# Kernel optimization log

Measured on AMD Instinct MI355X. Metric: run time of the kernel, lower is better.

## Reference

```python
import jax, jax.numpy as jnp
import numpy as np

U, I, NG, D, G, B = 100000, 50000, 20000, 64, 20, 16384
H_GE = (D + 2 * D) // 2  # 96, group_encoder hidden

def setup_inputs() -> dict:
    key = jax.random.key(0)
    ks = jax.random.split(key, 24)
    s = 0.1
    return {
        'group_inputs': jax.random.randint(ks[0], (B,), 0, NG),
        'item_inputs': jax.random.randint(ks[1], (B,), 0, I),
        'group_members': jax.random.randint(ks[2], (NG, G), 0, U),
        'eps': jax.random.normal(ks[3], (B, D), dtype=jnp.float32),
        'user_emb': jax.random.normal(ks[4], (U, D), dtype=jnp.float32) * s,
        'item_emb': jax.random.normal(ks[5], (I, D), dtype=jnp.float32) * s,
        # user_encoder: MLP(D, D, 1) -> Linear(D,D), ReLU, Linear(D,D)
        'ue_w1': jax.random.normal(ks[6], (D, D), dtype=jnp.float32) * s,
        'ue_b1': jnp.zeros((D,), jnp.float32),
        'ue_w2': jax.random.normal(ks[7], (D, D), dtype=jnp.float32) * s,
        'ue_b2': jnp.zeros((D,), jnp.float32),
        # group_encoder: MLP(D, 2D, 1) -> Linear(D,96), ReLU, Linear(96,2D)
        'ge_w1': jax.random.normal(ks[8], (D, H_GE), dtype=jnp.float32) * s,
        'ge_b1': jnp.zeros((H_GE,), jnp.float32),
        'ge_w2': jax.random.normal(ks[9], (H_GE, 2 * D), dtype=jnp.float32) * s,
        'ge_b2': jnp.zeros((2 * D,), jnp.float32),
        # attention: Linear(2D,16), ReLU, Linear(16,1)
        'at_w1': jax.random.normal(ks[10], (2 * D, 16), dtype=jnp.float32) * s,
        'at_b1': jnp.zeros((16,), jnp.float32),
        'at_w2': jax.random.normal(ks[11], (16, 1), dtype=jnp.float32) * s,
        'at_b2': jnp.zeros((1,), jnp.float32),
        # predict: Linear(3D,8), ReLU, Linear(8,1)
        'pr_w1': jax.random.normal(ks[12], (3 * D, 8), dtype=jnp.float32) * s,
        'pr_b1': jnp.zeros((8,), jnp.float32),
        'pr_w2': jax.random.normal(ks[13], (8, 1), dtype=jnp.float32) * s,
        'pr_b2': jnp.zeros((1,), jnp.float32),
    }

def reference(group_inputs, item_inputs, group_members, eps,
              user_emb, item_emb,
              ue_w1, ue_b1, ue_w2, ue_b2,
              ge_w1, ge_b1, ge_w2, ge_b2,
              at_w1, at_b1, at_w2, at_b2,
              pr_w1, pr_b1, pr_w2, pr_b2):
    mem_idx = group_members[group_inputs]              # [B, G]
    me = user_emb[mem_idx]                             # [B, G, D] gather
    # user encoder MLP
    enc = jnp.maximum(me @ ue_w1 + ue_b1, 0) @ ue_w2 + ue_b2
    gz = jnp.maximum(jnp.mean(enc, axis=1), 0)         # [B, D]
    gz = jnp.maximum(gz @ ge_w1 + ge_b1, 0) @ ge_w2 + ge_b2  # [B, 2D]
    z_mu, log_sigma = gz[:, :D], gz[:, D:]
    z_sigma = 0.1 + 0.9 * jax.nn.sigmoid(log_sigma)
    ie = item_emb[item_inputs]                          # [B, D]
    gi = jnp.concatenate([me, jnp.broadcast_to(ie[:, None, :], me.shape)], axis=-1)  # [B, G, 2D]
    score = jnp.maximum(gi @ at_w1 + at_b1, 0) @ at_w2 + at_b2  # [B, G, 1]
    w = jax.nn.softmax(score[..., 0], axis=1)           # [B, G]
    g_att = jnp.einsum('bg,bgd->bd', w, me)             # [B, D]
    ge_full = g_att + z_mu + z_sigma * eps              # sample_z with given eps
    ncf = jnp.concatenate([ge_full * ie, ge_full, ie], axis=-1)  # [B, 3D]
    h = jnp.maximum(ncf @ pr_w1 + pr_b1, 0) @ pr_w2 + pr_b2
    return jax.nn.sigmoid(h)                            # [B, 1]
```

## Files before the change

kernel.cpp:

```cpp
#include <hip/hip_runtime.h>
#include <hip/hip_bf16.h>
#include <math.h>

#define G_   20
#define BT   16

typedef __attribute__((ext_vector_type(8))) short bf8;
typedef __attribute__((ext_vector_type(4))) float f4;

#define FMB  0
#define FAT  10
#define FUE2 12
#define FGE1 20
#define FGE2 32
#define FPR  56
#define FTOT 62

__device__ __forceinline__ unsigned cvt2(float x, float y){
    float2 f; f.x = x; f.y = y;
    __hip_bfloat162 h = __float22bfloat162_rn(f);
    return *reinterpret_cast<unsigned*>(&h);
}
__device__ __forceinline__ unsigned short cvt1(float x){
    __hip_bfloat16 h = __float2bfloat16(x);
    return *reinterpret_cast<unsigned short*>(&h);
}
__device__ __forceinline__ bf8 pack8(float4 a, float4 b){
    union { bf8 v; unsigned u[4]; } t;
    t.u[0] = cvt2(a.x, a.y); t.u[1] = cvt2(a.z, a.w);
    t.u[2] = cvt2(b.x, b.y); t.u[3] = cvt2(b.z, b.w);
    return t.v;
}

__global__ __launch_bounds__(256) void vargr_prep(
    const float* __restrict__ ue_w1, const float* __restrict__ ue_w2,
    const float* __restrict__ ge_w1, const float* __restrict__ ge_w2,
    const float* __restrict__ at_w1, const float* __restrict__ pr_w1,
    unsigned short* __restrict__ ws)
{
    int f = blockIdx.x * 256 + threadIdx.x;
    if (f >= FTOT * 64) return;
    int lane = f & 63, grp = f >> 6;
    int col = lane & 15;
    int q8  = (lane >> 4) * 8;
    float v[8];
    if (grp < FAT){
        int g = grp - FMB; int nt = g >> 1; int k0 = (g & 1)*32 + q8; int c = nt*16 + col;
        #pragma unroll
        for (int q = 0; q < 8; ++q)
            v[q] = (c < 64) ? ue_w1[(k0+q)*64 + c] : at_w1[(k0+q)*16 + (c - 64)];
    } else if (grp < FUE2){
        int g = grp - FAT; int k0 = g*32 + q8;
        #pragma unroll
        for (int q = 0; q < 8; ++q) v[q] = at_w1[(64 + k0 + q)*16 + col];
    } else if (grp < FGE1){
        int g = grp - FUE2; int nt = g >> 1; int k0 = (g & 1)*32 + q8;
        #pragma unroll
        for (int q = 0; q < 8; ++q) v[q] = ue_w2[(k0+q)*64 + nt*16 + col];
    } else if (grp < FGE2){
        int g = grp - FGE1; int nt = g >> 1; int k0 = (g & 1)*32 + q8;
        #pragma unroll
        for (int q = 0; q < 8; ++q) v[q] = ge_w1[(k0+q)*96 + nt*16 + col];
    } else if (grp < FPR){
        int g = grp - FGE2; int nt = g / 3; int k0 = (g % 3)*32 + q8;
        #pragma unroll
        for (int q = 0; q < 8; ++q) v[q] = ge_w2[(k0+q)*128 + nt*16 + col];
    } else {
        int g = grp - FPR; int k0 = g*32 + q8;
        #pragma unroll
        for (int q = 0; q < 8; ++q) v[q] = (col < 8) ? pr_w1[(k0+q)*8 + col] : 0.f;
    }
    union { bf8 b; unsigned u[4]; } t;
    t.u[0] = cvt2(v[0], v[1]); t.u[1] = cvt2(v[2], v[3]);
    t.u[2] = cvt2(v[4], v[5]); t.u[3] = cvt2(v[6], v[7]);
    *reinterpret_cast<bf8*>(ws + (size_t)f * 8) = t.b;
}

__global__ __launch_bounds__(256, 4) void vargr_main(
    const int*   __restrict__ group_inputs,
    const int*   __restrict__ item_inputs,
    const int*   __restrict__ group_members,
    const float* __restrict__ eps,
    const float* __restrict__ user_emb,
    const float* __restrict__ item_emb,
    const float* __restrict__ ue_b1, const float* __restrict__ ue_b2,
    const float* __restrict__ ge_b1, const float* __restrict__ ge_b2,
    const float* __restrict__ at_b1, const float* __restrict__ at_w2,
    const float* __restrict__ at_b2, const float* __restrict__ pr_b1,
    const float* __restrict__ pr_w2, const float* __restrict__ pr_b2,
    const unsigned short* __restrict__ ws,
    float* __restrict__ out)
{
    __shared__ unsigned short xAh[BT*136];
    __shared__ unsigned short xBh[BT*136];
    __shared__ float ieb[BT*68];
    __shared__ float gefb[BT*64];
    __shared__ float wsm[BT*G_];
    __shared__ int   sidx[BT*G_];
    __shared__ float x3u[BT*132];

    const int tid = threadIdx.x;
    const int w = tid >> 6, l = tid & 63;
    const int lq = l >> 4, lr = l & 15;
    const int bbase = blockIdx.x * BT;
    const bf8* wsf = (const bf8*)ws;

    bf8 bfr[5][2];
    #pragma unroll
    for (int nt = 0; nt < 5; ++nt)
        #pragma unroll
        for (int kt = 0; kt < 2; ++kt)
            bfr[nt][kt] = wsf[(FMB + nt*2 + kt)*64 + l];
    bf8 abot0 = wsf[(FAT + 0)*64 + l];
    bf8 abot1 = wsf[(FAT + 1)*64 + l];

    float bias1[4];
    #pragma unroll
    for (int nt = 0; nt < 4; ++nt) bias1[nt] = ue_b1[nt*16 + lr];
    const float aw2  = at_w2[lr];
    const float atb2 = at_b2[0];

    {
        int bb = 4*w + lq;
        int item = item_inputs[bbase + bb];
        ((float4*)(ieb + bb*68))[lr] = ((const float4*)(item_emb + (size_t)item*64))[lr];
    }
    if (l < G_){
        #pragma unroll
        for (int i = 0; i < 4; ++i){
            int bb = 4*w + i;
            int gid = group_inputs[bbase + bb];
            sidx[bb*G_ + l] = group_members[gid*G_ + l];
        }
    }
    __syncthreads();

    f4 tvacc = (f4){0.f, 0.f, 0.f, 0.f};
    #pragma unroll
    for (int kt = 0; kt < 2; ++kt){
        const float* ap = ieb + lr*68 + kt*32 + lq*8;
        bf8 a = pack8(*(const float4*)ap, *(const float4*)(ap + 4));
        tvacc = __builtin_amdgcn_mfma_f32_16x16x32_bf16(a, kt ? abot1 : abot0, tvacc, 0, 0, 0);
    }
    const float atb1 = at_b1[lr];
    float tvi[4];
    #pragma unroll
    for (int i = 0; i < 4; ++i)
        tvi[i] = __shfl(tvacc[i], w*16 + lr) + atb1;

    float rem[4];
    {
        int sx = sidx[(4*w + (lr >> 2))*G_ + 16 + (lr & 3)];
        const float4* p = (const float4*)(user_emb + (size_t)sx*64) + lq*2;
        bf8 a0 = pack8(p[0], p[1]);
        bf8 a1 = pack8(p[8], p[9]);
        f4 acc[5];
        #pragma unroll
        for (int nt = 0; nt < 5; ++nt) acc[nt] = (f4){0.f, 0.f, 0.f, 0.f};
        #pragma unroll
        for (int nt = 0; nt < 5; ++nt){
            acc[nt] = __builtin_amdgcn_mfma_f32_16x16x32_bf16(a0, bfr[nt][0], acc[nt], 0, 0, 0);
            acc[nt] = __builtin_amdgcn_mfma_f32_16x16x32_bf16(a1, bfr[nt][1], acc[nt], 0, 0, 0);
        }
        #pragma unroll
        for (int nt = 0; nt < 4; ++nt){
            float rs = 0.f;
            #pragma unroll
            for (int rr = 0; rr < 4; ++rr) rs += fmaxf(acc[nt][rr] + bias1[nt], 0.f);
            rem[nt] = rs;
        }
        float tvq = (lq == 0) ? tvi[0] : (lq == 1) ? tvi[1] : (lq == 2) ? tvi[2] : tvi[3];
        float vv[4];
        #pragma unroll
        for (int rr = 0; rr < 4; ++rr) vv[rr] = fmaxf(acc[4][rr] + tvq, 0.f) * aw2;
        #pragma unroll
        for (int rr = 0; rr < 4; ++rr){
            vv[rr] += __shfl_xor(vv[rr], 1, 16);
            vv[rr] += __shfl_xor(vv[rr], 2, 16);
            vv[rr] += __shfl_xor(vv[rr], 4, 16);
            vv[rr] += __shfl_xor(vv[rr], 8, 16);
        }
        if (lr == 0){
            #pragma unroll
            for (int rr = 0; rr < 4; ++rr)
                wsm[(4*w + lq)*G_ + 16 + rr] = vv[rr] + atb2;
        }
    }

    #pragma unroll 1
    for (int i = 0; i < 4; ++i){
        const int bb = 4*w + i;
        const int sx = sidx[bb*G_ + lr];
        const float4* p = (const float4*)(user_emb + (size_t)sx*64) + lq*2;
        bf8 a0 = pack8(p[0], p[1]);
        bf8 a1 = pack8(p[8], p[9]);
        f4 acc[5];
        #pragma unroll
        for (int nt = 0; nt < 5; ++nt) acc[nt] = (f4){0.f, 0.f, 0.f, 0.f};
        #pragma unroll
        for (int nt = 0; nt < 5; ++nt){
            acc[nt] = __builtin_amdgcn_mfma_f32_16x16x32_bf16(a0, bfr[nt][0], acc[nt], 0, 0, 0);
            acc[nt] = __builtin_amdgcn_mfma_f32_16x16x32_bf16(a1, bfr[nt][1], acc[nt], 0, 0, 0);
        }
        #pragma unroll
        for (int nt = 0; nt < 4; ++nt){
            float rs = 0.f;
            #pragma unroll
            for (int rr = 0; rr < 4; ++rr) rs += fmaxf(acc[nt][rr] + bias1[nt], 0.f);
            if (lq == i) rs += rem[nt];
            rs += __shfl_xor(rs, 16);
            rs += __shfl_xor(rs, 32);
            if (lq == nt) xAh[bb*136 + nt*16 + lr] = cvt1(rs * (1.f / G_));
        }
        {
            float vv[4];
            #pragma unroll
            for (int rr = 0; rr < 4; ++rr) vv[rr] = fmaxf(acc[4][rr] + tvi[i], 0.f) * aw2;
            #pragma unroll
            for (int rr = 0; rr < 4; ++rr){
                vv[rr] += __shfl_xor(vv[rr], 1, 16);
                vv[rr] += __shfl_xor(vv[rr], 2, 16);
                vv[rr] += __shfl_xor(vv[rr], 4, 16);
                vv[rr] += __shfl_xor(vv[rr], 8, 16);
            }
            if (lr == 0){
                #pragma unroll
                for (int rr = 0; rr < 4; ++rr)
                    wsm[bb*G_ + 4*lq + rr] = vv[rr] + atb2;
            }
        }
        {
            float sval = (l < G_) ? wsm[bb*G_ + l] : -3.0e38f;
            float mx = sval;
            mx = fmaxf(mx, __shfl_xor(mx, 1, 32));
            mx = fmaxf(mx, __shfl_xor(mx, 2, 32));
            mx = fmaxf(mx, __shfl_xor(mx, 4, 32));
            mx = fmaxf(mx, __shfl_xor(mx, 8, 32));
            mx = fmaxf(mx, __shfl_xor(mx, 16, 32));
            float e = (l < G_) ? expf(sval - mx) : 0.f;
            float sm = e;
            sm += __shfl_xor(sm, 1, 32);
            sm += __shfl_xor(sm, 2, 32);
            sm += __shfl_xor(sm, 4, 32);
            sm += __shfl_xor(sm, 8, 32);
            sm += __shfl_xor(sm, 16, 32);
            if (l < G_) wsm[bb*G_ + l] = e / sm;
        }
        {
            float ga = 0.f;
            #pragma unroll
            for (int g = 0; g < G_; ++g)
                ga += wsm[bb*G_ + g] * user_emb[(size_t)sidx[bb*G_ + g]*64 + l];
            gefb[bb*64 + l] = ga;
        }
    }
    __syncthreads();

    {
        int col = w*16 + lr;
        f4 acc = (f4){0.f, 0.f, 0.f, 0.f};
        #pragma unroll
        for (int kt = 0; kt < 2; ++kt){
            bf8 a = *(const bf8*)(xAh + lr*136 + kt*32 + lq*8);
            acc = __builtin_amdgcn_mfma_f32_16x16x32_bf16(a, wsf[(FUE2 + w*2 + kt)*64 + l], acc, 0, 0, 0);
        }
        float bs = ue_b2[col];
        #pragma unroll
        for (int rr = 0; rr < 4; ++rr)
            xBh[(4*lq + rr)*136 + col] = cvt1(fmaxf(acc[rr] + bs, 0.f));
    }
    __syncthreads();
    for (int t = w; t < 6; t += 4){
        int col = t*16 + lr;
        f4 acc = (f4){0.f, 0.f, 0.f, 0.f};
        #pragma unroll
        for (int kt = 0; kt < 2; ++kt){
            bf8 a = *(const bf8*)(xBh + lr*136 + kt*32 + lq*8);
            acc = __builtin_amdgcn_mfma_f32_16x16x32_bf16(a, wsf[(FGE1 + t*2 + kt)*64 + l], acc, 0, 0, 0);
        }
        float bs = ge_b1[col];
        #pragma unroll
        for (int rr = 0; rr < 4; ++rr)
            xAh[(4*lq + rr)*136 + col] = cvt1(fmaxf(acc[rr] + bs, 0.f));
    }
    __syncthreads();
    for (int t = w; t < 8; t += 4){
        int col = t*16 + lr;
        f4 acc = (f4){0.f, 0.f, 0.f, 0.f};
        #pragma unroll
        for (int kt = 0; kt < 3; ++kt){
            bf8 a = *(const bf8*)(xAh + lr*136 + kt*32 + lq*8);
            acc = __builtin_amdgcn_mfma_f32_16x16x32_bf16(a, wsf[(FGE2 + t*3 + kt)*64 + l], acc, 0, 0, 0);
        }
        float bs = ge_b2[col];
        #pragma unroll
        for (int rr = 0; rr < 4; ++rr)
            x3u[(4*lq + rr)*132 + col] = acc[rr] + bs;
    }
    __syncthreads();

    #pragma unroll
    for (int i = 0; i < 4; ++i){
        int bb = 4*w + i;
        float mu  = x3u[bb*132 + l];
        float sgr = x3u[bb*132 + 64 + l];
        float sg  = 0.1f + 0.9f / (1.f + expf(-sgr));
        gefb[bb*64 + l] += mu + sg * eps[(size_t)(bbase + bb)*64 + l];
    }
    __syncthreads();
    unsigned short* ncf = (unsigned short*)x3u;
    #pragma unroll
    for (int i = 0; i < 4; ++i){
        int bb = 4*w + i;
        float gef = gefb[bb*64 + l];
        float iev = ieb[bb*68 + l];
        ncf[bb*200 + l]       = cvt1(gef * iev);
        ncf[bb*200 + 64 + l]  = cvt1(gef);
        ncf[bb*200 + 128 + l] = cvt1(iev);
    }
    __syncthreads();
    if (w == 0){
        f4 acc = (f4){0.f, 0.f, 0.f, 0.f};
        #pragma unroll
        for (int kt = 0; kt < 6; ++kt){
            bf8 a = *(const bf8*)(ncf + lr*200 + kt*32 + lq*8);
            acc = __builtin_amdgcn_mfma_f32_16x16x32_bf16(a, wsf[(FPR + kt)*64 + l], acc, 0, 0, 0);
        }
        float pb1 = (lr < 8) ? pr_b1[lr] : 0.f;
        float pw2 = (lr < 8) ? pr_w2[lr] : 0.f;
        float pb2 = pr_b2[0];
        float vv[4];
        #pragma unroll
        for (int rr = 0; rr < 4; ++rr) vv[rr] = fmaxf(acc[rr] + pb1, 0.f) * pw2;
        #pragma unroll
        for (int rr = 0; rr < 4; ++rr){
            vv[rr] += __shfl_xor(vv[rr], 1, 16);
            vv[rr] += __shfl_xor(vv[rr], 2, 16);
            vv[rr] += __shfl_xor(vv[rr], 4, 16);
            vv[rr] += __shfl_xor(vv[rr], 8, 16);
        }
        if (lr == 0){
            #pragma unroll
            for (int rr = 0; rr < 4; ++rr)
                out[bbase + 4*lq + rr] = 1.f / (1.f + expf(-(vv[rr] + pb2)));
        }
    }
}

extern "C" void kernel_launch(void* const* d_in, const int* in_sizes, int n_in,
                              void* d_out, int out_size, void* d_ws, size_t ws_size,
                              hipStream_t stream) {
    const int*   group_inputs  = (const int*)d_in[0];
    const int*   item_inputs   = (const int*)d_in[1];
    const int*   group_members = (const int*)d_in[2];
    const float* eps           = (const float*)d_in[3];
    const float* user_emb      = (const float*)d_in[4];
    const float* item_emb      = (const float*)d_in[5];
    const float* ue_w1 = (const float*)d_in[6];
    const float* ue_b1 = (const float*)d_in[7];
    const float* ue_w2 = (const float*)d_in[8];
    const float* ue_b2 = (const float*)d_in[9];
    const float* ge_w1 = (const float*)d_in[10];
    const float* ge_b1 = (const float*)d_in[11];
    const float* ge_w2 = (const float*)d_in[12];
    const float* ge_b2 = (const float*)d_in[13];
    const float* at_w1 = (const float*)d_in[14];
    const float* at_b1 = (const float*)d_in[15];
    const float* at_w2 = (const float*)d_in[16];
    const float* at_b2 = (const float*)d_in[17];
    const float* pr_w1 = (const float*)d_in[18];
    const float* pr_b1 = (const float*)d_in[19];
    const float* pr_w2 = (const float*)d_in[20];
    const float* pr_b2 = (const float*)d_in[21];
    float* out = (float*)d_out;
    unsigned short* ws = (unsigned short*)d_ws;

    vargr_prep<<<(FTOT*64 + 255)/256, 256, 0, stream>>>(
        ue_w1, ue_w2, ge_w1, ge_w2, at_w1, pr_w1, ws);

    const int nb = in_sizes[0];
    vargr_main<<<nb / BT, 256, 0, stream>>>(
        group_inputs, item_inputs, group_members, eps, user_emb, item_emb,
        ue_b1, ue_b2, ge_b1, ge_b2, at_b1, at_w2, at_b2, pr_b1, pr_w2, pr_b2,
        ws, out);
}
```

Baseline: 44.97 us.

## Double block tile to 32 rows and run tail MLP per-wave without barriers

Each block now handles 32 batch rows with 512 threads instead of 16 rows with 256 threads. After the gather and attention phase, only two waves continue, and each owns a 16-row slice. That wave runs the ue2, ge1, ge2, sampling and predict MLP chain alone, so the block-wide __syncthreads between tail stages go away, and eps is prefetched into registers early. The cost is that six of eight waves sit idle during the tail and register pressure rises. The diff also relies on the unseen shared-memory arrays being resized for BT=32.

```diff
diff --git a/kernel.cpp b/kernel.cpp
--- a/kernel.cpp
+++ b/kernel.cpp
@@ -3,7 +3,7 @@
 #include <math.h>
 
 #define G_   20
-#define BT   16
+#define BT   32
 
 typedef __attribute__((ext_vector_type(8))) short bf8;
 typedef __attribute__((ext_vector_type(4))) float f4;
@@ -76,7 +76,7 @@
     *reinterpret_cast<bf8*>(ws + (size_t)f * 8) = t.b;
 }
 
-__global__ __launch_bounds__(256, 4) void vargr_main(
+__global__ __launch_bounds__(512, 4) void vargr_main(
     const int*   __restrict__ group_inputs,
     const int*   __restrict__ item_inputs,
     const int*   __restrict__ group_members,
@@ -136,17 +136,20 @@
     __syncthreads();
 
     f4 tvacc = (f4){0.f, 0.f, 0.f, 0.f};
-    #pragma unroll
-    for (int kt = 0; kt < 2; ++kt){
-        const float* ap = ieb + lr*68 + kt*32 + lq*8;
-        bf8 a = pack8(*(const float4*)ap, *(const float4*)(ap + 4));
-        tvacc = __builtin_amdgcn_mfma_f32_16x16x32_bf16(a, kt ? abot1 : abot0, tvacc, 0, 0, 0);
+    {
+        int trow = ((w >> 2) << 4) + lr;
+        #pragma unroll
+        for (int kt = 0; kt < 2; ++kt){
+            const float* ap = ieb + trow*68 + kt*32 + lq*8;
+            bf8 a = pack8(*(const float4*)ap, *(const float4*)(ap + 4));
+            tvacc = __builtin_amdgcn_mfma_f32_16x16x32_bf16(a, kt ? abot1 : abot0, tvacc, 0, 0, 0);
+        }
     }
     const float atb1 = at_b1[lr];
     float tvi[4];
     #pragma unroll
     for (int i = 0; i < 4; ++i)
-        tvi[i] = __shfl(tvacc[i], w*16 + lr) + atb1;
+        tvi[i] = __shfl(tvacc[i], ((w & 3) << 4) + lr) + atb1;
 
     float rem[4];
     {
@@ -254,72 +257,79 @@
             gefb[bb*64 + l] = ga;
         }
     }
+
     __syncthreads();
-
-    {
-        int col = w*16 + lr;
+    if (w >= 2) return;
+
+    const int base = 16 * w;
+
+    float ev[16];
+    #pragma unroll
+    for (int j = 0; j < 16; ++j)
+        ev[j] = eps[(size_t)(bbase + base + j)*64 + l];
+
+    #pragma unroll
+    for (int nt = 0; nt < 4; ++nt){
+        int col = nt*16 + lr;
         f4 acc = (f4){0.f, 0.f, 0.f, 0.f};
         #pragma unroll
         for (int kt = 0; kt < 2; ++kt){
-            bf8 a = *(const bf8*)(xAh + lr*136 + kt*32 + lq*8);
-            acc = __builtin_amdgcn_mfma_f32_16x16x32_bf16(a, wsf[(FUE2 + w*2 + kt)*64 + l], acc, 0, 0, 0);
+            bf8 a = *(const bf8*)(xAh + (base + lr)*136 + kt*32 + lq*8);
+            acc = __builtin_amdgcn_mfma_f32_16x16x32_bf16(a, wsf[(FUE2 + nt*2 + kt)*64 + l], acc, 0, 0, 0);
         }
         float bs = ue_b2[col];
         #pragma unroll
         for (int rr = 0; rr < 4; ++rr)
-            xBh[(4*lq + rr)*136 + col] = cvt1(fmaxf(acc[rr] + bs, 0.f));
-    }
-    __syncthreads();
-    for (int t = w; t < 6; t += 4){
+            xBh[(base + 4*lq + rr)*136 + col] = cvt1(fmaxf(acc[rr] + bs, 0.f));
+    }
+    #pragma unroll
+    for (int t = 0; t < 6; ++t){
         int col = t*16 + lr;
         f4 acc = (f4){0.f, 0.f, 0.f, 0.f};
         #pragma unroll
         for (int kt = 0; kt < 2; ++kt){
-            bf8 a = *(const bf8*)(xBh + lr*136 + kt*32 + lq*8);
+            bf8 a = *(const bf8*)(xBh + (base + lr)*136 + kt*32 + lq*8);
             acc = __builtin_amdgcn_mfma_f32_16x16x32_bf16(a, wsf[(FGE1 + t*2 + kt)*64 + l], acc, 0, 0, 0);
         }
         float bs = ge_b1[col];
         #pragma unroll
         for (int rr = 0; rr < 4; ++rr)
-            xAh[(4*lq + rr)*136 + col] = cvt1(fmaxf(acc[rr] + bs, 0.f));
-    }
-    __syncthreads();
-    for (int t = w; t < 8; t += 4){
+            xAh[(base + 4*lq + rr)*136 + col] = cvt1(fmaxf(acc[rr] + bs, 0.f));
+    }
+    #pragma unroll
+    for (int t = 0; t < 8; ++t){
         int col = t*16 + lr;
         f4 acc = (f4){0.f, 0.f, 0.f, 0.f};
         #pragma unroll
         for (int kt = 0; kt < 3; ++kt){
-            bf8 a = *(const bf8*)(xAh + lr*136 + kt*32 + lq*8);
+            bf8 a = *(const bf8*)(xAh + (base + lr)*136 + kt*32 + lq*8);
             acc = __builtin_amdgcn_mfma_f32_16x16x32_bf16(a, wsf[(FGE2 + t*3 + kt)*64 + l], acc, 0, 0, 0);
         }
         float bs = ge_b2[col];
         #pragma unroll
         for (int rr = 0; rr < 4; ++rr)
-            x3u[(4*lq + rr)*132 + col] = acc[rr] + bs;
-    }
-    __syncthreads();
-
-    #pragma unroll
-    for (int i = 0; i < 4; ++i){
-        int bb = 4*w + i;
-        float mu  = x3u[bb*132 + l];
-        float sgr = x3u[bb*132 + 64 + l];
+            x3u[(base + 4*lq + rr)*132 + col] = acc[rr] + bs;
+    }
+
+    float gefv[16];
+    #pragma unroll
+    for (int j = 0; j < 16; ++j){
+        float mu  = x3u[(base + j)*132 + l];
+        float sgr = x3u[(base + j)*132 + 64 + l];
         float sg  = 0.1f + 0.9f / (1.f + expf(-sgr));
-        gefb[bb*64 + l] += mu + sg * eps[(size_t)(bbase + bb)*64 + l];
-    }
-    __syncthreads();
-    unsigned short* ncf = (unsigned short*)x3u;
-    #pragma unroll
-    for (int i = 0; i < 4; ++i){
-        int bb = 4*w + i;
-        float gef = gefb[bb*64 + l];
-        float iev = ieb[bb*68 + l];
-        ncf[bb*200 + l]       = cvt1(gef * iev);
-        ncf[bb*200 + 64 + l]  = cvt1(gef);
-        ncf[bb*200 + 128 + l] = cvt1(iev);
-    }
-    __syncthreads();
-    if (w == 0){
+        gefv[j] = gefb[(base + j)*64 + l] + mu + sg * ev[j];
+    }
+    asm volatile("" ::: "memory");
+    unsigned short* ncf = (unsigned short*)x3u + (size_t)base * 264;
+    #pragma unroll
+    for (int j = 0; j < 16; ++j){
+        float gef = gefv[j];
+        float iev = ieb[(base + j)*68 + l];
+        ncf[j*200 + l]       = cvt1(gef * iev);
+        ncf[j*200 + 64 + l]  = cvt1(gef);
+        ncf[j*200 + 128 + l] = cvt1(iev);
+    }
+    {
         f4 acc = (f4){0.f, 0.f, 0.f, 0.f};
         #pragma unroll
         for (int kt = 0; kt < 6; ++kt){
@@ -342,7 +352,7 @@
         if (lr == 0){
             #pragma unroll
             for (int rr = 0; rr < 4; ++rr)
-                out[bbase + 4*lq + rr] = 1.f / (1.f + expf(-(vv[rr] + pb2)));
+                out[bbase + base + 4*lq + rr] = 1.f / (1.f + expf(-(vv[rr] + pb2)));
         }
     }
 }
@@ -379,7 +389,7 @@
         ue_w1, ue_w2, ge_w1, ge_w2, at_w1, pr_w1, ws);
 
     const int nb = in_sizes[0];
-    vargr_main<<<nb / BT, 256, 0, stream>>>(
+    vargr_main<<<nb / BT, 512, 0, stream>>>(
         group_inputs, item_inputs, group_members, eps, user_emb, item_emb,
         ue_b1, ue_b2, ge_b1, ge_b2, at_b1, at_w2, at_b2, pr_b1, pr_w2, pr_b2,
         ws, out);
```

New measurement: 52.99 us. +17.9%, slower.

## Use one wavefront per batch row with 1024-thread blocks and single-wave tail

Applied to the files above, without the earlier changes.

Grows the block from 4 to 16 wavefronts so each wavefront handles one batch row's 20 members. The member and remainder embedding rows are loaded up front, before the barrier, so gather latency overlaps the other setup work. After one barrier, the small group-encoder and predict MLP chain runs entirely in wavefront 0 without further block barriers, and eps is prefetched into registers. This raises parallelism and removes the serial per-row loop and several barriers. In exchange, 15 of the 16 wavefronts idle during the tail, and register pressure under launch_bounds(1024) may limit occupancy.

```diff
diff --git a/kernel.cpp b/kernel.cpp
--- a/kernel.cpp
+++ b/kernel.cpp
@@ -76,7 +76,7 @@
     *reinterpret_cast<bf8*>(ws + (size_t)f * 8) = t.b;
 }
 
-__global__ __launch_bounds__(256, 4) void vargr_main(
+__global__ __launch_bounds__(1024, 4) void vargr_main(
     const int*   __restrict__ group_inputs,
     const int*   __restrict__ item_inputs,
     const int*   __restrict__ group_members,
@@ -91,18 +91,19 @@
     const unsigned short* __restrict__ ws,
     float* __restrict__ out)
 {
-    __shared__ unsigned short xAh[BT*136];
-    __shared__ unsigned short xBh[BT*136];
     __shared__ float ieb[BT*68];
-    __shared__ float gefb[BT*64];
     __shared__ float wsm[BT*G_];
     __shared__ int   sidx[BT*G_];
+    __shared__ unsigned short xAh[BT*136];
+    __shared__ float gefb[BT*64];
+    __shared__ unsigned short xBh[BT*136];
     __shared__ float x3u[BT*132];
 
     const int tid = threadIdx.x;
     const int w = tid >> 6, l = tid & 63;
     const int lq = l >> 4, lr = l & 15;
     const int bbase = blockIdx.x * BT;
+    const int bb = w;
     const bf8* wsf = (const bf8*)ws;
 
     bf8 bfr[5][2];
@@ -119,60 +120,73 @@
     for (int nt = 0; nt < 4; ++nt) bias1[nt] = ue_b1[nt*16 + lr];
     const float aw2  = at_w2[lr];
     const float atb2 = at_b2[0];
-
-    {
-        int bb = 4*w + lq;
+    const float atb1 = at_b1[lr];
+
+    {
         int item = item_inputs[bbase + bb];
-        ((float4*)(ieb + bb*68))[lr] = ((const float4*)(item_emb + (size_t)item*64))[lr];
-    }
-    if (l < G_){
-        #pragma unroll
-        for (int i = 0; i < 4; ++i){
-            int bb = 4*w + i;
-            int gid = group_inputs[bbase + bb];
-            sidx[bb*G_ + l] = group_members[gid*G_ + l];
-        }
-    }
+        if (l < 16)
+            ((float4*)(ieb + bb*68))[l] = ((const float4*)(item_emb + (size_t)item*64))[l];
+        int gid = group_inputs[bbase + bb];
+        if (l < G_) sidx[bb*G_ + l] = group_members[gid*G_ + l];
+    }
+
+    bf8 a0, a1, b0, b1;
+    {
+        int sxm = sidx[bb*G_ + lr];
+        const float4* pm = (const float4*)(user_emb + (size_t)sxm*64) + lq*2;
+        float4 m0 = pm[0], m1 = pm[1], m2 = pm[8], m3 = pm[9];
+        int rr2 = (lr < 4) ? lr : 3;
+        int sxr = sidx[bb*G_ + 16 + rr2];
+        const float4* pr_ = (const float4*)(user_emb + (size_t)sxr*64) + lq*2;
+        float4 q0 = pr_[0], q1 = pr_[1], q2 = pr_[8], q3 = pr_[9];
+        a0 = pack8(m0, m1); a1 = pack8(m2, m3);
+        b0 = pack8(q0, q1); b1 = pack8(q2, q3);
+    }
+
     __syncthreads();
 
-    f4 tvacc = (f4){0.f, 0.f, 0.f, 0.f};
-    #pragma unroll
-    for (int kt = 0; kt < 2; ++kt){
-        const float* ap = ieb + lr*68 + kt*32 + lq*8;
-        bf8 a = pack8(*(const float4*)ap, *(const float4*)(ap + 4));
-        tvacc = __builtin_amdgcn_mfma_f32_16x16x32_bf16(a, kt ? abot1 : abot0, tvacc, 0, 0, 0);
-    }
-    const float atb1 = at_b1[lr];
-    float tvi[4];
-    #pragma unroll
-    for (int i = 0; i < 4; ++i)
-        tvi[i] = __shfl(tvacc[i], w*16 + lr) + atb1;
-
-    float rem[4];
-    {
-        int sx = sidx[(4*w + (lr >> 2))*G_ + 16 + (lr & 3)];
-        const float4* p = (const float4*)(user_emb + (size_t)sx*64) + lq*2;
-        bf8 a0 = pack8(p[0], p[1]);
-        bf8 a1 = pack8(p[8], p[9]);
-        f4 acc[5];
-        #pragma unroll
-        for (int nt = 0; nt < 5; ++nt) acc[nt] = (f4){0.f, 0.f, 0.f, 0.f};
-        #pragma unroll
-        for (int nt = 0; nt < 5; ++nt){
-            acc[nt] = __builtin_amdgcn_mfma_f32_16x16x32_bf16(a0, bfr[nt][0], acc[nt], 0, 0, 0);
-            acc[nt] = __builtin_amdgcn_mfma_f32_16x16x32_bf16(a1, bfr[nt][1], acc[nt], 0, 0, 0);
-        }
-        #pragma unroll
-        for (int nt = 0; nt < 4; ++nt){
-            float rs = 0.f;
+    float tvi;
+    {
+        f4 tvacc = (f4){0.f, 0.f, 0.f, 0.f};
+        #pragma unroll
+        for (int kt = 0; kt < 2; ++kt){
+            const float* ap = ieb + lr*68 + kt*32 + lq*8;
+            bf8 a = pack8(*(const float4*)ap, *(const float4*)(ap + 4));
+            tvacc = __builtin_amdgcn_mfma_f32_16x16x32_bf16(a, kt ? abot1 : abot0, tvacc, 0, 0, 0);
+        }
+        int wm = w & 3;
+        float src = (wm == 0) ? tvacc[0] : (wm == 1) ? tvacc[1] : (wm == 2) ? tvacc[2] : tvacc[3];
+        tvi = __shfl(src, (w >> 2)*16 + lr) + atb1;
+    }
+
+    f4 accM[5], accR[5];
+    #pragma unroll
+    for (int nt = 0; nt < 5; ++nt){ accM[nt] = (f4){0.f,0.f,0.f,0.f}; accR[nt] = (f4){0.f,0.f,0.f,0.f}; }
+    #pragma unroll
+    for (int nt = 0; nt < 5; ++nt){
+        accM[nt] = __builtin_amdgcn_mfma_f32_16x16x32_bf16(a0, bfr[nt][0], accM[nt], 0, 0, 0);
+        accM[nt] = __builtin_amdgcn_mfma_f32_16x16x32_bf16(a1, bfr[nt][1], accM[nt], 0, 0, 0);
+        accR[nt] = __builtin_amdgcn_mfma_f32_16x16x32_bf16(b0, bfr[nt][0], accR[nt], 0, 0, 0);
+        accR[nt] = __builtin_amdgcn_mfma_f32_16x16x32_bf16(b1, bfr[nt][1], accR[nt], 0, 0, 0);
+    }
+
+    #pragma unroll
+    for (int nt = 0; nt < 4; ++nt){
+        float rs = 0.f;
+        #pragma unroll
+        for (int rr = 0; rr < 4; ++rr) rs += fmaxf(accM[nt][rr] + bias1[nt], 0.f);
+        if (lq == 0){
             #pragma unroll
-            for (int rr = 0; rr < 4; ++rr) rs += fmaxf(acc[nt][rr] + bias1[nt], 0.f);
-            rem[nt] = rs;
-        }
-        float tvq = (lq == 0) ? tvi[0] : (lq == 1) ? tvi[1] : (lq == 2) ? tvi[2] : tvi[3];
+            for (int rr = 0; rr < 4; ++rr) rs += fmaxf(accR[nt][rr] + bias1[nt], 0.f);
+        }
+        rs += __shfl_xor(rs, 16);
+        rs += __shfl_xor(rs, 32);
+        if (lq == nt) xAh[bb*136 + nt*16 + lr] = cvt1(rs * (1.f / G_));
+    }
+    {
         float vv[4];
         #pragma unroll
-        for (int rr = 0; rr < 4; ++rr) vv[rr] = fmaxf(acc[4][rr] + tvq, 0.f) * aw2;
+        for (int rr = 0; rr < 4; ++rr) vv[rr] = fmaxf(accM[4][rr] + tvi, 0.f) * aw2;
         #pragma unroll
         for (int rr = 0; rr < 4; ++rr){
             vv[rr] += __shfl_xor(vv[rr], 1, 16);
@@ -182,95 +196,74 @@
         }
         if (lr == 0){
             #pragma unroll
-            for (int rr = 0; rr < 4; ++rr)
-                wsm[(4*w + lq)*G_ + 16 + rr] = vv[rr] + atb2;
-        }
-    }
-
-    #pragma unroll 1
-    for (int i = 0; i < 4; ++i){
-        const int bb = 4*w + i;
-        const int sx = sidx[bb*G_ + lr];
-        const float4* p = (const float4*)(user_emb + (size_t)sx*64) + lq*2;
-        bf8 a0 = pack8(p[0], p[1]);
-        bf8 a1 = pack8(p[8], p[9]);
-        f4 acc[5];
-        #pragma unroll
-        for (int nt = 0; nt < 5; ++nt) acc[nt] = (f4){0.f, 0.f, 0.f, 0.f};
-        #pragma unroll
-        for (int nt = 0; nt < 5; ++nt){
-            acc[nt] = __builtin_amdgcn_mfma_f32_16x16x32_bf16(a0, bfr[nt][0], acc[nt], 0, 0, 0);
-            acc[nt] = __builtin_amdgcn_mfma_f32_16x16x32_bf16(a1, bfr[nt][1], acc[nt], 0, 0, 0);
-        }
-        #pragma unroll
-        for (int nt = 0; nt < 4; ++nt){
-            float rs = 0.f;
+            for (int rr = 0; rr < 4; ++rr) wsm[bb*G_ + 4*lq + rr] = vv[rr] + atb2;
+        }
+        float vr[4];
+        #pragma unroll
+        for (int rr = 0; rr < 4; ++rr) vr[rr] = fmaxf(accR[4][rr] + tvi, 0.f) * aw2;
+        #pragma unroll
+        for (int rr = 0; rr < 4; ++rr){
+            vr[rr] += __shfl_xor(vr[rr], 1, 16);
+            vr[rr] += __shfl_xor(vr[rr], 2, 16);
+            vr[rr] += __shfl_xor(vr[rr], 4, 16);
+            vr[rr] += __shfl_xor(vr[rr], 8, 16);
+        }
+        if (lq == 0 && lr == 0){
             #pragma unroll
-            for (int rr = 0; rr < 4; ++rr) rs += fmaxf(acc[nt][rr] + bias1[nt], 0.f);
-            if (lq == i) rs += rem[nt];
-            rs += __shfl_xor(rs, 16);
-            rs += __shfl_xor(rs, 32);
-            if (lq == nt) xAh[bb*136 + nt*16 + lr] = cvt1(rs * (1.f / G_));
-        }
-        {
-            float vv[4];
-            #pragma unroll
-            for (int rr = 0; rr < 4; ++rr) vv[rr] = fmaxf(acc[4][rr] + tvi[i], 0.f) * aw2;
-            #pragma unroll
-            for (int rr = 0; rr < 4; ++rr){
-                vv[rr] += __shfl_xor(vv[rr], 1, 16);
-                vv[rr] += __shfl_xor(vv[rr], 2, 16);
-                vv[rr] += __shfl_xor(vv[rr], 4, 16);
-                vv[rr] += __shfl_xor(vv[rr], 8, 16);
-            }
-            if (lr == 0){
-                #pragma unroll
-                for (int rr = 0; rr < 4; ++rr)
-                    wsm[bb*G_ + 4*lq + rr] = vv[rr] + atb2;
-            }
-        }
-        {
-            float sval = (l < G_) ? wsm[bb*G_ + l] : -3.0e38f;
-            float mx = sval;
-            mx = fmaxf(mx, __shfl_xor(mx, 1, 32));
-            mx = fmaxf(mx, __shfl_xor(mx, 2, 32));
-            mx = fmaxf(mx, __shfl_xor(mx, 4, 32));
-            mx = fmaxf(mx, __shfl_xor(mx, 8, 32));
-            mx = fmaxf(mx, __shfl_xor(mx, 16, 32));
-            float e = (l < G_) ? expf(sval - mx) : 0.f;
-            float sm = e;
-            sm += __shfl_xor(sm, 1, 32);
-            sm += __shfl_xor(sm, 2, 32);
-            sm += __shfl_xor(sm, 4, 32);
-            sm += __shfl_xor(sm, 8, 32);
-            sm += __shfl_xor(sm, 16, 32);
-            if (l < G_) wsm[bb*G_ + l] = e / sm;
-        }
-        {
-            float ga = 0.f;
-            #pragma unroll
-            for (int g = 0; g < G_; ++g)
-                ga += wsm[bb*G_ + g] * user_emb[(size_t)sidx[bb*G_ + g]*64 + l];
-            gefb[bb*64 + l] = ga;
-        }
-    }
+            for (int rr = 0; rr < 4; ++rr) wsm[bb*G_ + 16 + rr] = vr[rr] + atb2;
+        }
+    }
+    {
+        float sval = (l < G_) ? wsm[bb*G_ + l] : -3.0e38f;
+        float mx = sval;
+        mx = fmaxf(mx, __shfl_xor(mx, 1, 32));
+        mx = fmaxf(mx, __shfl_xor(mx, 2, 32));
+        mx = fmaxf(mx, __shfl_xor(mx, 4, 32));
+        mx = fmaxf(mx, __shfl_xor(mx, 8, 32));
+        mx = fmaxf(mx, __shfl_xor(mx, 16, 32));
+        float e = (l < G_) ? expf(sval - mx) : 0.f;
+        float sm = e;
+        sm += __shfl_xor(sm, 1, 32);
+        sm += __shfl_xor(sm, 2, 32);
+        sm += __shfl_xor(sm, 4, 32);
+        sm += __shfl_xor(sm, 8, 32);
+        sm += __shfl_xor(sm, 16, 32);
+        if (l < G_) wsm[bb*G_ + l] = e / sm;
+    }
+    {
+        float ga = 0.f;
+        #pragma unroll
+        for (int g = 0; g < G_; ++g)
+            ga += wsm[bb*G_ + g] * user_emb[(size_t)sidx[bb*G_ + g]*64 + l];
+        gefb[bb*64 + l] = ga;
+    }
+
+    float ev[16];
+    if (w == 0){
+        #pragma unroll
+        for (int j = 0; j < 16; ++j)
+            ev[j] = eps[(size_t)(bbase + j)*64 + l];
+    }
+
     __syncthreads();
-
-    {
-        int col = w*16 + lr;
+    if (w != 0) return;
+
+    #pragma unroll
+    for (int nt = 0; nt < 4; ++nt){
+        int col = nt*16 + lr;
         f4 acc = (f4){0.f, 0.f, 0.f, 0.f};
         #pragma unroll
         for (int kt = 0; kt < 2; ++kt){
             bf8 a = *(const bf8*)(xAh + lr*136 + kt*32 + lq*8);
-            acc = __builtin_amdgcn_mfma_f32_16x16x32_bf16(a, wsf[(FUE2 + w*2 + kt)*64 + l], acc, 0, 0, 0);
+            acc = __builtin_amdgcn_mfma_f32_16x16x32_bf16(a, wsf[(FUE2 + nt*2 + kt)*64 + l], acc, 0, 0, 0);
         }
         float bs = ue_b2[col];
         #pragma unroll
         for (int rr = 0; rr < 4; ++rr)
             xBh[(4*lq + rr)*136 + col] = cvt1(fmaxf(acc[rr] + bs, 0.f));
     }
-    __syncthreads();
-    for (int t = w; t < 6; t += 4){
+    #pragma unroll
+    for (int t = 0; t < 6; ++t){
         int col = t*16 + lr;
         f4 acc = (f4){0.f, 0.f, 0.f, 0.f};
         #pragma unroll
@@ -283,8 +276,8 @@
         for (int rr = 0; rr < 4; ++rr)
             xAh[(4*lq + rr)*136 + col] = cvt1(fmaxf(acc[rr] + bs, 0.f));
     }
-    __syncthreads();
-    for (int t = w; t < 8; t += 4){
+    #pragma unroll
+    for (int t = 0; t < 8; ++t){
         int col = t*16 + lr;
         f4 acc = (f4){0.f, 0.f, 0.f, 0.f};
         #pragma unroll
@@ -297,29 +290,26 @@
         for (int rr = 0; rr < 4; ++rr)
             x3u[(4*lq + rr)*132 + col] = acc[rr] + bs;
     }
-    __syncthreads();
-
-    #pragma unroll
-    for (int i = 0; i < 4; ++i){
-        int bb = 4*w + i;
-        float mu  = x3u[bb*132 + l];
-        float sgr = x3u[bb*132 + 64 + l];
+
+    float gefv[BT];
+    #pragma unroll
+    for (int j = 0; j < BT; ++j){
+        float mu  = x3u[j*132 + l];
+        float sgr = x3u[j*132 + 64 + l];
         float sg  = 0.1f + 0.9f / (1.f + expf(-sgr));
-        gefb[bb*64 + l] += mu + sg * eps[(size_t)(bbase + bb)*64 + l];
-    }
-    __syncthreads();
+        gefv[j] = gefb[j*64 + l] + mu + sg * ev[j];
+    }
+    asm volatile("" ::: "memory");
     unsigned short* ncf = (unsigned short*)x3u;
     #pragma unroll
-    for (int i = 0; i < 4; ++i){
-        int bb = 4*w + i;
-        float gef = gefb[bb*64 + l];
-        float iev = ieb[bb*68 + l];
-        ncf[bb*200 + l]       = cvt1(gef * iev);
-        ncf[bb*200 + 64 + l]  = cvt1(gef);
-        ncf[bb*200 + 128 + l] = cvt1(iev);
-    }
-    __syncthreads();
-    if (w == 0){
+    for (int j = 0; j < BT; ++j){
+        float g  = gefv[j];
+        float ie = ieb[j*68 + l];
+        ncf[j*200 + l]       = cvt1(g * ie);
+        ncf[j*200 + 64 + l]  = cvt1(g);
+        ncf[j*200 + 128 + l] = cvt1(ie);
+    }
+    {
         f4 acc = (f4){0.f, 0.f, 0.f, 0.f};
         #pragma unroll
         for (int kt = 0; kt < 6; ++kt){
@@ -379,7 +369,7 @@
         ue_w1, ue_w2, ge_w1, ge_w2, at_w1, pr_w1, ws);
 
     const int nb = in_sizes[0];
-    vargr_main<<<nb / BT, 256, 0, stream>>>(
+    vargr_main<<<nb / BT, 1024, 0, stream>>>(
         group_inputs, item_inputs, group_members, eps, user_emb, item_emb,
         ue_b1, ue_b2, ge_b1, ge_b2, at_b1, at_w2, at_b2, pr_b1, pr_w2, pr_b2,
         ws, out);
```

Measured after the change: 66.65 us. 48.2% more time.
